# Kernel tuning notes

Measured on AMD Instinct MI355X. Metric: run time of the kernel, lower is better.

Reference implementation:

```python
import jax, jax.numpy as jnp
import numpy as np

LEAKY_SLOPE = 0.2  # tf.nn.leaky_relu default alpha
L2_EPS = 1e-12     # tf.nn.l2_normalize default epsilon


def setup_inputs() -> dict:
    key = jax.random.key(0)
    N, d, E, k = 100000, 64, 1600000, 3
    k0, k1, k2, k3 = jax.random.split(key, 4)
    x = jax.random.normal(k0, (N, d), dtype=jnp.float32)
    edge_index = jax.random.randint(k1, (2, E), 0, N, dtype=jnp.int32)
    scale = 1.0 / np.sqrt(d).astype(np.float32)
    W_gcn = jax.random.normal(k2, (k, d, d), dtype=jnp.float32) * scale
    W_int = jax.random.normal(k3, (k, d, d), dtype=jnp.float32) * scale
    b_gcn = jnp.zeros((k, d), dtype=jnp.float32)
    b_int = jnp.zeros((k, d), dtype=jnp.float32)
    return {"x": x, "edge_index": edge_index, "W_gcn": W_gcn, "b_gcn": b_gcn,
            "W_int": W_int, "b_int": b_int}


def _l2norm(h):
    sq = jnp.sum(h * h, axis=-1, keepdims=True)
    return h * jax.lax.rsqrt(jnp.maximum(sq, L2_EPS))


def reference(x, edge_index, W_gcn, b_gcn, W_int, b_int):
    N = x.shape[0]
    row, col = edge_index[0], edge_index[1]
    # LightGCN.norm_adj: symmetric normalization D^-1/2 A D^-1/2 (no self-loops)
    deg = jax.ops.segment_sum(jnp.ones_like(row, dtype=x.dtype), row, num_segments=N)
    dinv = jnp.where(deg > 0, jax.lax.rsqrt(deg), 0.0)
    w = dinv[row] * dinv[col]  # [E]

    def agg(h):
        # sparse normed_adj @ h : gather source feats, scale, scatter-add to dst
        return jax.ops.segment_sum(w[:, None] * h[col], row, num_segments=N)

    lrelu = lambda z: jax.nn.leaky_relu(z, LEAKY_SLOPE)
    h = x
    outs = [x]
    for i in range(W_gcn.shape[0]):
        ha = agg(h)  # [N, d]
        h = lrelu(ha @ W_gcn[i] + b_gcn[i]) + lrelu((h * ha) @ W_int[i] + b_int[i])
        outs.append(_l2norm(h))
    return jnp.concatenate(outs, axis=-1)  # [N, (k+1)*d]
```

## Files before the change

### kernel.cpp

```cpp
#include <hip/hip_runtime.h>


#define LEAKY 0.2f
#define NBK_MAX 512
#define TILE_A 4096
#define BCAP 5120

typedef unsigned short ushort_t;
typedef short short8 __attribute__((ext_vector_type(8)));
typedef float f32x4 __attribute__((ext_vector_type(4)));

__device__ __forceinline__ float lrelu(float z) { return z > 0.f ? z : LEAKY * z; }

__device__ __forceinline__ unsigned f2bf(float f) {
  unsigned u = __float_as_uint(f);
  return (u + 0x7FFFu + ((u >> 16) & 1u)) >> 16;
}

__device__ __forceinline__ float bf2f(unsigned u) {
  return __uint_as_float(u << 16);
}

__device__ __forceinline__ int rfl(const int* p) {
  return __builtin_amdgcn_readfirstlane(*p);
}

__global__ __launch_bounds__(256) void zerotails_k(int* __restrict__ tails, int nbk) {
  int t = blockIdx.x * 256 + threadIdx.x;
  if (t < nbk) tails[t] = 0;
}

__global__ __launch_bounds__(256) void bucket_k(const int* __restrict__ row,
                                                const int* __restrict__ col,
                                                int* __restrict__ tails,
                                                unsigned int* __restrict__ buckets,
                                                int E, int nbk) {
  __shared__ int bcnt[NBK_MAX], bex[NBK_MAX], bnext[NBK_MAX], gbase[NBK_MAX];
  __shared__ int ssc[256];
  int t = threadIdx.x;
  int ts = blockIdx.x * TILE_A;
  int tn = E - ts;
  if (tn > TILE_A) tn = TILE_A;
  bcnt[t] = 0;
  bcnt[t + 256] = 0;
  __syncthreads();
  for (int i = t; i < tn; i += 256) atomicAdd(&bcnt[row[ts + i] >> 8], 1);
  __syncthreads();
  int a0 = bcnt[2 * t], a1 = bcnt[2 * t + 1];
  ssc[t] = a0 + a1;
  __syncthreads();
  #pragma unroll
  for (int off = 1; off < 256; off <<= 1) {
    int x = (t >= off) ? ssc[t - off] : 0;
    __syncthreads();
    ssc[t] += x;
    __syncthreads();
  }
  int ex = ssc[t] - (a0 + a1);
  bex[2 * t] = ex;
  bex[2 * t + 1] = ex + a0;
  bnext[2 * t] = ex;
  bnext[2 * t + 1] = ex + a0;
  if (t < nbk && bcnt[t] > 0) gbase[t] = atomicAdd(&tails[t], bcnt[t]);
  int t2 = t + 256;
  if (t2 < nbk && bcnt[t2] > 0) gbase[t2] = atomicAdd(&tails[t2], bcnt[t2]);
  __syncthreads();
  for (int i = t; i < tn; i += 256) {
    int r = row[ts + i], c = col[ts + i];
    int b = r >> 8;
    int k = atomicAdd(&bnext[b], 1) - bex[b];
    int pos = gbase[b] + k;
    if (pos < BCAP)
      buckets[(size_t)b * BCAP + pos] = ((unsigned)(r & 255) << 24) | (unsigned)c;
  }
}

__global__ __launch_bounds__(512) void bkscan_k(const int* __restrict__ tails,
                                                int* __restrict__ bkbase,
                                                int* __restrict__ rp,
                                                int nbk, int N, int E) {
  __shared__ int s[512];
  int t = threadIdx.x;
  int v = (t < nbk) ? tails[t] : 0;
  s[t] = v;
  __syncthreads();
  #pragma unroll
  for (int off = 1; off < 512; off <<= 1) {
    int x = (t >= off) ? s[t - off] : 0;
    __syncthreads();
    s[t] += x;
    __syncthreads();
  }
  if (t < nbk) bkbase[t] = s[t] - v;
  if (t == 0) rp[N] = E;
}

__global__ __launch_bounds__(256) void csr_k(const int* __restrict__ tails,
                                             const int* __restrict__ bkbase,
                                             const unsigned int* __restrict__ buckets,
                                             int* __restrict__ rp,
                                             float* __restrict__ dinv,
                                             int* __restrict__ packed, int N) {
  __shared__ int cnt[256], sc[256], cnt2[256];
  int b = blockIdx.x, t = threadIdx.x;
  int row0 = b << 8;
  int nrows = N - row0;
  if (nrows > 256) nrows = 256;
  int cb = tails[b];
  if (cb > BCAP) cb = BCAP;
  int base = bkbase[b];
  const unsigned int* ent = buckets + (size_t)b * BCAP;
  cnt[t] = 0;
  __syncthreads();
  for (int i = t; i < cb; i += 256) atomicAdd(&cnt[ent[i] >> 24], 1);
  __syncthreads();
  int v = cnt[t];
  sc[t] = v;
  __syncthreads();
  #pragma unroll
  for (int off = 1; off < 256; off <<= 1) {
    int x = (t >= off) ? sc[t - off] : 0;
    __syncthreads();
    sc[t] += x;
    __syncthreads();
  }
  int ex = sc[t] - v;
  if (t < nrows) {
    rp[row0 + t] = base + ex;
    dinv[row0 + t] = (v > 0) ? rsqrtf((float)v) : 0.f;
  }
  cnt[t] = ex;
  cnt2[t] = 0;
  __syncthreads();
  for (int i = t; i < cb; i += 256) {
    unsigned e = ent[i];
    int rl = e >> 24;
    int slot = atomicAdd(&cnt2[rl], 1);
    packed[base + cnt[rl] + slot] = (int)(e & 0xFFFFFFu);
  }
}

__global__ __launch_bounds__(256) void copyx_k(const float* __restrict__ x,
                                               const float* __restrict__ dinv,
                                               float* __restrict__ out,
                                               ushort_t* __restrict__ xb,
                                               ushort_t* __restrict__ xg,
                                               int N, int ostride4) {
  int total = N * 16;
  int stride = gridDim.x * blockDim.x;
  for (int i = blockIdx.x * blockDim.x + threadIdx.x; i < total; i += stride) {
    int n = i >> 4, c4 = i & 15;
    float4 v = ((const float4*)x)[i];
    ((float4*)out)[(size_t)n * ostride4 + c4] = v;
    unsigned p0 = f2bf(v.x) | (f2bf(v.y) << 16);
    unsigned p1 = f2bf(v.z) | (f2bf(v.w) << 16);
    ((uint2*)xb)[i] = make_uint2(p0, p1);
    float dv = dinv[n];
    unsigned q0 = f2bf(v.x * dv) | (f2bf(v.y * dv) << 16);
    unsigned q1 = f2bf(v.z * dv) | (f2bf(v.w * dv) << 16);
    ((uint2*)xg)[i] = make_uint2(q0, q1);
  }
}

__global__ __launch_bounds__(256) void packw_k(const float* __restrict__ Wg,
                                               const float* __restrict__ Wi,
                                               ushort_t* __restrict__ Wfrag,
                                               int total) {
  int tid = blockIdx.x * 256 + threadIdx.x;
  if (tid >= total) return;
  int lane = tid & 63;
  int kh = (tid >> 6) & 1;
  int nt = (tid >> 7) & 3;
  int gm = (tid >> 9) & 1;
  int ly = tid >> 10;
  const float* W = (gm ? Wi : Wg) + (size_t)ly * 4096;
  int kb = (kh << 5) + ((lane >> 4) << 3);
  int n = (nt << 4) + (lane & 15);
  unsigned u[4];
  #pragma unroll
  for (int j = 0; j < 4; ++j) {
    unsigned lo = f2bf(W[(kb + 2 * j) * 64 + n]);
    unsigned hi = f2bf(W[(kb + 2 * j + 1) * 64 + n]);
    u[j] = lo | (hi << 16);
  }
  ((uint4*)Wfrag)[tid] = make_uint4(u[0], u[1], u[2], u[3]);
}

__global__ __launch_bounds__(256) void agg_k(const int* __restrict__ rp,
                                             const int* __restrict__ packed,
                                             const float* __restrict__ dinv,
                                             const ushort_t* __restrict__ gin,
                                             ushort_t* __restrict__ ha, int N) {
  int wv = (((blockIdx.x << 2) + (threadIdx.x >> 6)) << 1);
  if (wv >= N) return;
  int lane = threadIdx.x & 63;
  int grp = lane >> 3;
  int l8 = lane & 7;
  bool have1 = (wv + 1) < N;
  int s0 = rfl(&rp[wv]);
  int e0 = rfl(&rp[wv + 1]);
  int s1 = have1 ? rfl(&rp[wv + 1]) : 0;
  int e1 = have1 ? rfl(&rp[wv + 2]) : 0;
  float dr0 = __int_as_float(__builtin_amdgcn_readfirstlane(__float_as_int(dinv[wv])));
  float dr1 = have1 ? __int_as_float(__builtin_amdgcn_readfirstlane(
                          __float_as_int(dinv[wv + 1])))
                    : 0.f;
  float a0[8], a1[8];
  #pragma unroll
  for (int i = 0; i < 8; ++i) { a0[i] = 0.f; a1[i] = 0.f; }
  int bidx0 = grp << 2;
  int ch0 = s0, ch1 = s1;
  while (ch0 < e0 || ch1 < e1) {
    int m0 = e0 - ch0;
    if (m0 > 64) m0 = 64;
    int m1 = e1 - ch1;
    if (m1 > 64) m1 = 64;
    int cl0 = (m0 > 0 && lane < m0) ? packed[ch0 + lane] : 0;
    int cl1 = (m1 > 0 && lane < m1) ? packed[ch1 + lane] : 0;
    int mm = m0 > m1 ? m0 : m1;
    int nit = (mm + 7) >> 3;
    #pragma unroll 2
    for (int j = 0; j < nit; ++j) {
      int bi = bidx0 + (j << 5);
      int c0 = __builtin_amdgcn_ds_bpermute(bi, cl0);
      int c1 = __builtin_amdgcn_ds_bpermute(bi, cl1);
      int eidx = (j << 3) + grp;
      float msk0 = (eidx < m0) ? 1.f : 0.f;
      float msk1 = (eidx < m1) ? 1.f : 0.f;
      uint4 v0 = ((const uint4*)(gin + ((size_t)c0 << 6)))[l8];
      uint4 v1 = ((const uint4*)(gin + ((size_t)c1 << 6)))[l8];
      a0[0] = fmaf(msk0, bf2f(v0.x & 0xFFFFu), a0[0]);
      a0[1] = fmaf(msk0, bf2f(v0.x >> 16), a0[1]);
      a0[2] = fmaf(msk0, bf2f(v0.y & 0xFFFFu), a0[2]);
      a0[3] = fmaf(msk0, bf2f(v0.y >> 16), a0[3]);
      a0[4] = fmaf(msk0, bf2f(v0.z & 0xFFFFu), a0[4]);
      a0[5] = fmaf(msk0, bf2f(v0.z >> 16), a0[5]);
      a0[6] = fmaf(msk0, bf2f(v0.w & 0xFFFFu), a0[6]);
      a0[7] = fmaf(msk0, bf2f(v0.w >> 16), a0[7]);
      a1[0] = fmaf(msk1, bf2f(v1.x & 0xFFFFu), a1[0]);
      a1[1] = fmaf(msk1, bf2f(v1.x >> 16), a1[1]);
      a1[2] = fmaf(msk1, bf2f(v1.y & 0xFFFFu), a1[2]);
      a1[3] = fmaf(msk1, bf2f(v1.y >> 16), a1[3]);
      a1[4] = fmaf(msk1, bf2f(v1.z & 0xFFFFu), a1[4]);
      a1[5] = fmaf(msk1, bf2f(v1.z >> 16), a1[5]);
      a1[6] = fmaf(msk1, bf2f(v1.w & 0xFFFFu), a1[6]);
      a1[7] = fmaf(msk1, bf2f(v1.w >> 16), a1[7]);
    }
    ch0 += 64;
    ch1 += 64;
  }
  #pragma unroll
  for (int off = 8; off < 64; off <<= 1)
    #pragma unroll
    for (int i = 0; i < 8; ++i) {
      a0[i] += __shfl_xor(a0[i], off);
      a1[i] += __shfl_xor(a1[i], off);
    }
  if (grp == 0) {
    unsigned u0 = f2bf(a0[0] * dr0) | (f2bf(a0[1] * dr0) << 16);
    unsigned u1 = f2bf(a0[2] * dr0) | (f2bf(a0[3] * dr0) << 16);
    unsigned u2 = f2bf(a0[4] * dr0) | (f2bf(a0[5] * dr0) << 16);
    unsigned u3 = f2bf(a0[6] * dr0) | (f2bf(a0[7] * dr0) << 16);
    ((uint4*)(ha + ((size_t)wv << 6)))[l8] = make_uint4(u0, u1, u2, u3);
  } else if (grp == 1 && have1) {
    unsigned u0 = f2bf(a1[0] * dr1) | (f2bf(a1[1] * dr1) << 16);
    unsigned u1 = f2bf(a1[2] * dr1) | (f2bf(a1[3] * dr1) << 16);
    unsigned u2 = f2bf(a1[4] * dr1) | (f2bf(a1[5] * dr1) << 16);
    unsigned u3 = f2bf(a1[6] * dr1) | (f2bf(a1[7] * dr1) << 16);
    ((uint4*)(ha + ((size_t)(wv + 1) << 6)))[l8] = make_uint4(u0, u1, u2, u3);
  }
}

__global__ __launch_bounds__(256) void gemmM_k(const ushort_t* __restrict__ ha,
                                               const ushort_t* __restrict__ hin,
                                               const ushort_t* __restrict__ Wfrag,
                                               const float* __restrict__ bg,
                                               const float* __restrict__ bi,
                                               const float* __restrict__ dinv,
                                               ushort_t* __restrict__ hout,
                                               ushort_t* __restrict__ gout,
                                               float* __restrict__ outp,
                                               int N, int ntiles, int ostride) {
  int lane = threadIdx.x & 63;
  int gq = lane >> 4, ln15 = lane & 15;
  const short8* wf = (const short8*)Wfrag;
  short8 bG[8], bI[8];
  #pragma unroll
  for (int nt = 0; nt < 4; ++nt)
    #pragma unroll
    for (int kh = 0; kh < 2; ++kh) {
      bG[nt * 2 + kh] = wf[nt * 128 + kh * 64 + lane];
      bI[nt * 2 + kh] = wf[512 + nt * 128 + kh * 64 + lane];
    }
  float bgv[4], biv[4];
  #pragma unroll
  for (int nt = 0; nt < 4; ++nt) {
    bgv[nt] = bg[nt * 16 + ln15];
    biv[nt] = bi[nt * 16 + ln15];
  }
  int wid = (blockIdx.x << 2) + (threadIdx.x >> 6);
  int nw = gridDim.x << 2;
  for (int tile = wid; tile < ntiles; tile += nw) {
    int node0 = tile << 4;
    const short8* pa =
        (const short8*)(ha + (size_t)(node0 + ln15) * 64 + gq * 8);
    const short8* ph =
        (const short8*)(hin + (size_t)(node0 + ln15) * 64 + gq * 8);
    f32x4 acc1[4], acc2[4];
    #pragma unroll
    for (int nt = 0; nt < 4; ++nt) {
      acc1[nt] = (f32x4){bgv[nt], bgv[nt], bgv[nt], bgv[nt]};
      acc2[nt] = (f32x4){biv[nt], biv[nt], biv[nt], biv[nt]};
    }
    #pragma unroll
    for (int kh = 0; kh < 2; ++kh) {
      short8 af = pa[kh * 4];
      short8 hf = ph[kh * 4];
      short8 vmf;
      #pragma unroll
      for (int e2 = 0; e2 < 8; ++e2) {
        float fa = bf2f((ushort_t)af[e2]);
        float fh = bf2f((ushort_t)hf[e2]);
        vmf[e2] = (short)f2bf(fa * fh);
      }
      #pragma unroll
      for (int nt = 0; nt < 4; ++nt) {
        acc1[nt] = __builtin_amdgcn_mfma_f32_16x16x32_bf16(af, bG[nt * 2 + kh],
                                                           acc1[nt], 0, 0, 0);
        acc2[nt] = __builtin_amdgcn_mfma_f32_16x16x32_bf16(vmf, bI[nt * 2 + kh],
                                                           acc2[nt], 0, 0, 0);
      }
    }
    float z[4][4];
    float ssr[4] = {0.f, 0.f, 0.f, 0.f};
    #pragma unroll
    for (int nt = 0; nt < 4; ++nt)
      #pragma unroll
      for (int reg = 0; reg < 4; ++reg) {
        float zz = lrelu(acc1[nt][reg]) + lrelu(acc2[nt][reg]);
        z[nt][reg] = zz;
        ssr[reg] = fmaf(zz, zz, ssr[reg]);
      }
    #pragma unroll
    for (int off = 1; off < 16; off <<= 1)
      #pragma unroll
      for (int reg = 0; reg < 4; ++reg) ssr[reg] += __shfl_xor(ssr[reg], off);
    float inv[4];
    #pragma unroll
    for (int reg = 0; reg < 4; ++reg)
      inv[reg] = rsqrtf(fmaxf(ssr[reg], 1e-12f));
    #pragma unroll
    for (int reg = 0; reg < 4; ++reg) {
      int r = node0 + 4 * gq + reg;
      if (r < N) {
        float dv = dinv[r];
        #pragma unroll
        for (int nt = 0; nt < 4; ++nt) {
          outp[(size_t)r * ostride + nt * 16 + ln15] = z[nt][reg] * inv[reg];
          hout[(size_t)r * 64 + nt * 16 + ln15] = (ushort_t)f2bf(z[nt][reg]);
          gout[(size_t)r * 64 + nt * 16 + ln15] =
              (ushort_t)f2bf(z[nt][reg] * dv);
        }
      }
    }
  }
}

extern "C" void kernel_launch(void* const* d_in, const int* in_sizes, int n_in,
                              void* d_out, int out_size, void* d_ws, size_t ws_size,
                              hipStream_t stream) {
  const float* x  = (const float*)d_in[0];
  const int*   ei = (const int*)d_in[1];
  const float* Wg = (const float*)d_in[2];
  const float* bg = (const float*)d_in[3];
  const float* Wi = (const float*)d_in[4];
  const float* bi = (const float*)d_in[5];
  float* out = (float*)d_out;

  const int d = 64;
  const int N = in_sizes[0] / d;
  const int E = in_sizes[1] / 2;
  const int K = in_sizes[2] / (d * d);
  const int* row = ei;
  const int* col = ei + E;
  const int nbk = (N + 255) / 256;
  const int N16 = (N + 15) & ~15;
  const int ntiles = N16 / 16;
  const int ostride = (K + 1) * d;

  char* ws = (char*)d_ws;
  size_t off = 0;
  auto alloc = [&](size_t bytes) {
    char* p = ws + off;
    off = (off + bytes + 255) & ~(size_t)255;
    return p;
  };
  int*   tails  = (int*)alloc((size_t)NBK_MAX * 4);
  int*   bkbase = (int*)alloc((size_t)NBK_MAX * 4);
  int*   rp     = (int*)alloc((size_t)(N + 1) * 4);
  float* dinv   = (float*)alloc((size_t)N * 4);
  unsigned int* buckets = (unsigned int*)alloc((size_t)nbk * BCAP * 4);
  int*   packed = (int*)alloc((size_t)E * 4);
  ushort_t* ha  = (ushort_t*)alloc((size_t)N16 * d * 2);
  ushort_t* hb0 = (ushort_t*)alloc((size_t)N16 * d * 2);
  ushort_t* hb1 = (ushort_t*)alloc((size_t)N16 * d * 2);
  ushort_t* xb  = (ushort_t*)alloc((size_t)N16 * d * 2);
  ushort_t* hg0 = (ushort_t*)alloc((size_t)N16 * d * 2);
  ushort_t* hg1 = (ushort_t*)alloc((size_t)N16 * d * 2);
  ushort_t* xg  = (ushort_t*)alloc((size_t)N16 * d * 2);
  ushort_t* Wfrag = (ushort_t*)alloc((size_t)K * 8192 * 2);
  (void)ws_size;

  zerotails_k<<<(nbk + 255) / 256, 256, 0, stream>>>(tails, nbk);
  int ntA = (E + TILE_A - 1) / TILE_A;
  bucket_k<<<ntA, 256, 0, stream>>>(row, col, tails, buckets, E, nbk);
  bkscan_k<<<1, 512, 0, stream>>>(tails, bkbase, rp, nbk, N, E);
  csr_k<<<nbk, 256, 0, stream>>>(tails, bkbase, buckets, rp, dinv, packed, N);
  copyx_k<<<2048, 256, 0, stream>>>(x, dinv, out, xb, xg, N, ostride / 4);
  int wtotal = K * 1024;
  packw_k<<<(wtotal + 255) / 256, 256, 0, stream>>>(Wg, Wi, Wfrag, wtotal);

  const ushort_t* hin = xb;
  const ushort_t* gin = xg;
  ushort_t* hbufs[2] = {hb0, hb1};
  ushort_t* gbufs[2] = {hg0, hg1};
  int aggblocks = (N + 7) / 8;
  for (int i = 0; i < K; ++i) {
    ushort_t* hout = hbufs[i & 1];
    ushort_t* gout = gbufs[i & 1];
    agg_k<<<aggblocks, 256, 0, stream>>>(rp, packed, dinv, gin, ha, N);
    gemmM_k<<<1024, 256, 0, stream>>>(
        ha, hin, Wfrag + (size_t)i * 8192, bg + (size_t)i * d,
        bi + (size_t)i * d, dinv, hout, gout, out + (size_t)(i + 1) * d,
        N, ntiles, ostride);
    hin = hout;
    gin = gout;
  }
}
```

Baseline: 229.7 us.

## Drop unscaled bf16 h buffers, recover h from scaled copy, fuse x copy into CSR

The unscaled bf16 feature buffer is no longer stored. The GEMM kernel rebuilds h by multiplying the dinv-scaled copy by 1/dinv, which removes one bf16 write per layer and one read. The x copy and bf16 conversion move into csr_k, which uses a shared-memory dinv, so copyx_k and its extra launch go away. The edge-bucketing tile size doubles and the GEMM grid is sized to one tile per wave. The risks are extra rounding error from the bf16 round trip through scaling, and zero-degree rows losing their h value (rdv=0), which changes the h*ha term for nodes that have no out-edges.

After: 231.4 us. Within noise of the previous version (+0.8%).

```diff
diff --git a/kernel.cpp b/kernel.cpp
--- a/kernel.cpp
+++ b/kernel.cpp
@@ -3,7 +3,7 @@
 
 #define LEAKY 0.2f
 #define NBK_MAX 512
-#define TILE_A 4096
+#define TILE_A 8192
 #define BCAP 5120
 
 typedef unsigned short ushort_t;
@@ -100,8 +100,13 @@
                                              const unsigned int* __restrict__ buckets,
                                              int* __restrict__ rp,
                                              float* __restrict__ dinv,
-                                             int* __restrict__ packed, int N) {
+                                             int* __restrict__ packed,
+                                             const float* __restrict__ x,
+                                             float* __restrict__ out,
+                                             ushort_t* __restrict__ xg,
+                                             int N, int ostride4) {
   __shared__ int cnt[256], sc[256], cnt2[256];
+  __shared__ float sdinv[256];
   int b = blockIdx.x, t = threadIdx.x;
   int row0 = b << 8;
   int nrows = N - row0;
@@ -119,15 +124,17 @@
   __syncthreads();
   #pragma unroll
   for (int off = 1; off < 256; off <<= 1) {
-    int x = (t >= off) ? sc[t - off] : 0;
-    __syncthreads();
-    sc[t] += x;
+    int x2 = (t >= off) ? sc[t - off] : 0;
+    __syncthreads();
+    sc[t] += x2;
     __syncthreads();
   }
   int ex = sc[t] - v;
+  float dvv = (v > 0) ? rsqrtf((float)v) : 0.f;
+  sdinv[t] = dvv;
   if (t < nrows) {
     rp[row0 + t] = base + ex;
-    dinv[row0 + t] = (v > 0) ? rsqrtf((float)v) : 0.f;
+    dinv[row0 + t] = dvv;
   }
   cnt[t] = ex;
   cnt2[t] = 0;
@@ -138,27 +145,16 @@
     int slot = atomicAdd(&cnt2[rl], 1);
     packed[base + cnt[rl] + slot] = (int)(e & 0xFFFFFFu);
   }
-}
-
-__global__ __launch_bounds__(256) void copyx_k(const float* __restrict__ x,
-                                               const float* __restrict__ dinv,
-                                               float* __restrict__ out,
-                                               ushort_t* __restrict__ xb,
-                                               ushort_t* __restrict__ xg,
-                                               int N, int ostride4) {
-  int total = N * 16;
-  int stride = gridDim.x * blockDim.x;
-  for (int i = blockIdx.x * blockDim.x + threadIdx.x; i < total; i += stride) {
-    int n = i >> 4, c4 = i & 15;
-    float4 v = ((const float4*)x)[i];
-    ((float4*)out)[(size_t)n * ostride4 + c4] = v;
-    unsigned p0 = f2bf(v.x) | (f2bf(v.y) << 16);
-    unsigned p1 = f2bf(v.z) | (f2bf(v.w) << 16);
-    ((uint2*)xb)[i] = make_uint2(p0, p1);
-    float dv = dinv[n];
-    unsigned q0 = f2bf(v.x * dv) | (f2bf(v.y * dv) << 16);
-    unsigned q1 = f2bf(v.z * dv) | (f2bf(v.w * dv) << 16);
-    ((uint2*)xg)[i] = make_uint2(q0, q1);
+  int base4 = row0 << 4;
+  int tot4 = nrows << 4;
+  for (int i = t; i < tot4; i += 256) {
+    int rl = i >> 4, c4 = i & 15;
+    float4 vx = ((const float4*)x)[base4 + i];
+    ((float4*)out)[(size_t)(row0 + rl) * ostride4 + c4] = vx;
+    float dv = sdinv[rl];
+    unsigned q0 = f2bf(vx.x * dv) | (f2bf(vx.y * dv) << 16);
+    unsigned q1 = f2bf(vx.z * dv) | (f2bf(vx.w * dv) << 16);
+    ((uint2*)xg)[base4 + i] = make_uint2(q0, q1);
   }
 }
 
@@ -272,12 +268,11 @@
 }
 
 __global__ __launch_bounds__(256) void gemmM_k(const ushort_t* __restrict__ ha,
-                                               const ushort_t* __restrict__ hin,
+                                               const ushort_t* __restrict__ gin,
                                                const ushort_t* __restrict__ Wfrag,
                                                const float* __restrict__ bg,
                                                const float* __restrict__ bi,
                                                const float* __restrict__ dinv,
-                                               ushort_t* __restrict__ hout,
                                                ushort_t* __restrict__ gout,
                                                float* __restrict__ outp,
                                                int N, int ntiles, int ostride) {
@@ -302,10 +297,11 @@
   int nw = gridDim.x << 2;
   for (int tile = wid; tile < ntiles; tile += nw) {
     int node0 = tile << 4;
-    const short8* pa =
-        (const short8*)(ha + (size_t)(node0 + ln15) * 64 + gq * 8);
-    const short8* ph =
-        (const short8*)(hin + (size_t)(node0 + ln15) * 64 + gq * 8);
+    int r15 = node0 + ln15;
+    float dnv = dinv[r15];
+    float rdv = (dnv > 0.f) ? 1.f / dnv : 0.f;
+    const short8* pa = (const short8*)(ha + (size_t)r15 * 64 + gq * 8);
+    const short8* ph = (const short8*)(gin + (size_t)r15 * 64 + gq * 8);
     f32x4 acc1[4], acc2[4];
     #pragma unroll
     for (int nt = 0; nt < 4; ++nt) {
@@ -315,12 +311,12 @@
     #pragma unroll
     for (int kh = 0; kh < 2; ++kh) {
       short8 af = pa[kh * 4];
-      short8 hf = ph[kh * 4];
+      short8 gf = ph[kh * 4];
       short8 vmf;
       #pragma unroll
       for (int e2 = 0; e2 < 8; ++e2) {
         float fa = bf2f((ushort_t)af[e2]);
-        float fh = bf2f((ushort_t)hf[e2]);
+        float fh = bf2f((ushort_t)gf[e2]) * rdv;
         vmf[e2] = (short)f2bf(fa * fh);
       }
       #pragma unroll
@@ -357,7 +353,6 @@
         #pragma unroll
         for (int nt = 0; nt < 4; ++nt) {
           outp[(size_t)r * ostride + nt * 16 + ln15] = z[nt][reg] * inv[reg];
-          hout[(size_t)r * 64 + nt * 16 + ln15] = (ushort_t)f2bf(z[nt][reg]);
           gout[(size_t)r * 64 + nt * 16 + ln15] =
               (ushort_t)f2bf(z[nt][reg] * dv);
         }
@@ -398,13 +393,10 @@
   int*   tails  = (int*)alloc((size_t)NBK_MAX * 4);
   int*   bkbase = (int*)alloc((size_t)NBK_MAX * 4);
   int*   rp     = (int*)alloc((size_t)(N + 1) * 4);
-  float* dinv   = (float*)alloc((size_t)N * 4);
+  float* dinv   = (float*)alloc((size_t)N16 * 4);
   unsigned int* buckets = (unsigned int*)alloc((size_t)nbk * BCAP * 4);
   int*   packed = (int*)alloc((size_t)E * 4);
   ushort_t* ha  = (ushort_t*)alloc((size_t)N16 * d * 2);
-  ushort_t* hb0 = (ushort_t*)alloc((size_t)N16 * d * 2);
-  ushort_t* hb1 = (ushort_t*)alloc((size_t)N16 * d * 2);
-  ushort_t* xb  = (ushort_t*)alloc((size_t)N16 * d * 2);
   ushort_t* hg0 = (ushort_t*)alloc((size_t)N16 * d * 2);
   ushort_t* hg1 = (ushort_t*)alloc((size_t)N16 * d * 2);
   ushort_t* xg  = (ushort_t*)alloc((size_t)N16 * d * 2);
@@ -415,25 +407,22 @@
   int ntA = (E + TILE_A - 1) / TILE_A;
   bucket_k<<<ntA, 256, 0, stream>>>(row, col, tails, buckets, E, nbk);
   bkscan_k<<<1, 512, 0, stream>>>(tails, bkbase, rp, nbk, N, E);
-  csr_k<<<nbk, 256, 0, stream>>>(tails, bkbase, buckets, rp, dinv, packed, N);
-  copyx_k<<<2048, 256, 0, stream>>>(x, dinv, out, xb, xg, N, ostride / 4);
+  csr_k<<<nbk, 256, 0, stream>>>(tails, bkbase, buckets, rp, dinv, packed,
+                                 x, out, xg, N, ostride / 4);
   int wtotal = K * 1024;
   packw_k<<<(wtotal + 255) / 256, 256, 0, stream>>>(Wg, Wi, Wfrag, wtotal);
 
-  const ushort_t* hin = xb;
   const ushort_t* gin = xg;
-  ushort_t* hbufs[2] = {hb0, hb1};
   ushort_t* gbufs[2] = {hg0, hg1};
   int aggblocks = (N + 7) / 8;
+  int gemmblocks = (ntiles + 3) / 4;
   for (int i = 0; i < K; ++i) {
-    ushort_t* hout = hbufs[i & 1];
     ushort_t* gout = gbufs[i & 1];
     agg_k<<<aggblocks, 256, 0, stream>>>(rp, packed, dinv, gin, ha, N);
-    gemmM_k<<<1024, 256, 0, stream>>>(
-        ha, hin, Wfrag + (size_t)i * 8192, bg + (size_t)i * d,
-        bi + (size_t)i * d, dinv, hout, gout, out + (size_t)(i + 1) * d,
+    gemmM_k<<<gemmblocks, 256, 0, stream>>>(
+        ha, gin, Wfrag + (size_t)i * 8192, bg + (size_t)i * d,
+        bi + (size_t)i * d, dinv, gout, out + (size_t)(i + 1) * d,
         N, ntiles, ostride);
-    hin = hout;
     gin = gout;
   }
 }
```

## Store gathered neighbor features in FP8 to halve aggregation gather bandwidth

Applied to the files above, without the earlier changes.

The dinv-scaled feature copies that the aggregation kernel gathers per edge are now stored as FP8 (e4m3) instead of bf16. The kernel decodes them with packed FP8-to-float conversions, which halves the bytes fetched per random row gather. The last layer skips writing the gather buffer because no later layer reads it. The tail-zeroing kernel is folded into the weight-packing kernel to save a launch. The main risk is accuracy: FP8 gives about 3 mantissa bits and a limited range, which may exceed the output tolerance.

Result: faster. 223.7 us (-2.6%).

```diff
diff --git a/kernel.cpp b/kernel.cpp
--- a/kernel.cpp
+++ b/kernel.cpp
@@ -7,8 +7,10 @@
 #define BCAP 5120
 
 typedef unsigned short ushort_t;
+typedef unsigned char uchar_t;
 typedef short short8 __attribute__((ext_vector_type(8)));
 typedef float f32x4 __attribute__((ext_vector_type(4)));
+typedef float f32x2 __attribute__((ext_vector_type(2)));
 
 __device__ __forceinline__ float lrelu(float z) { return z > 0.f ? z : LEAKY * z; }
 
@@ -21,13 +23,12 @@
   return __uint_as_float(u << 16);
 }
 
+__device__ __forceinline__ unsigned f2fp8(float f) {
+  return (unsigned)__builtin_amdgcn_cvt_pk_fp8_f32(f, f, 0, false) & 0xFFu;
+}
+
 __device__ __forceinline__ int rfl(const int* p) {
   return __builtin_amdgcn_readfirstlane(*p);
-}
-
-__global__ __launch_bounds__(256) void zerotails_k(int* __restrict__ tails, int nbk) {
-  int t = blockIdx.x * 256 + threadIdx.x;
-  if (t < nbk) tails[t] = 0;
 }
 
 __global__ __launch_bounds__(256) void bucket_k(const int* __restrict__ row,
@@ -144,7 +145,7 @@
                                                const float* __restrict__ dinv,
                                                float* __restrict__ out,
                                                ushort_t* __restrict__ xb,
-                                               ushort_t* __restrict__ xg,
+                                               uchar_t* __restrict__ xg,
                                                int N, int ostride4) {
   int total = N * 16;
   int stride = gridDim.x * blockDim.x;
@@ -156,17 +157,21 @@
     unsigned p1 = f2bf(v.z) | (f2bf(v.w) << 16);
     ((uint2*)xb)[i] = make_uint2(p0, p1);
     float dv = dinv[n];
-    unsigned q0 = f2bf(v.x * dv) | (f2bf(v.y * dv) << 16);
-    unsigned q1 = f2bf(v.z * dv) | (f2bf(v.w * dv) << 16);
-    ((uint2*)xg)[i] = make_uint2(q0, q1);
+    unsigned pkA =
+        (unsigned)__builtin_amdgcn_cvt_pk_fp8_f32(v.x * dv, v.y * dv, 0, false);
+    unsigned pkB =
+        (unsigned)__builtin_amdgcn_cvt_pk_fp8_f32(v.z * dv, v.w * dv, 0, false);
+    ((unsigned*)xg)[i] = (pkA & 0xFFFFu) | ((pkB & 0xFFFFu) << 16);
   }
 }
 
 __global__ __launch_bounds__(256) void packw_k(const float* __restrict__ Wg,
                                                const float* __restrict__ Wi,
                                                ushort_t* __restrict__ Wfrag,
-                                               int total) {
+                                               int total,
+                                               int* __restrict__ tails, int nbk) {
   int tid = blockIdx.x * 256 + threadIdx.x;
+  if (tid < nbk) tails[tid] = 0;
   if (tid >= total) return;
   int lane = tid & 63;
   int kh = (tid >> 6) & 1;
@@ -189,7 +194,7 @@
 __global__ __launch_bounds__(256) void agg_k(const int* __restrict__ rp,
                                              const int* __restrict__ packed,
                                              const float* __restrict__ dinv,
-                                             const ushort_t* __restrict__ gin,
+                                             const uchar_t* __restrict__ gin,
                                              ushort_t* __restrict__ ha, int N) {
   int wv = (((blockIdx.x << 2) + (threadIdx.x >> 6)) << 1);
   if (wv >= N) return;
@@ -227,24 +232,25 @@
       int eidx = (j << 3) + grp;
       float msk0 = (eidx < m0) ? 1.f : 0.f;
       float msk1 = (eidx < m1) ? 1.f : 0.f;
-      uint4 v0 = ((const uint4*)(gin + ((size_t)c0 << 6)))[l8];
-      uint4 v1 = ((const uint4*)(gin + ((size_t)c1 << 6)))[l8];
-      a0[0] = fmaf(msk0, bf2f(v0.x & 0xFFFFu), a0[0]);
-      a0[1] = fmaf(msk0, bf2f(v0.x >> 16), a0[1]);
-      a0[2] = fmaf(msk0, bf2f(v0.y & 0xFFFFu), a0[2]);
-      a0[3] = fmaf(msk0, bf2f(v0.y >> 16), a0[3]);
-      a0[4] = fmaf(msk0, bf2f(v0.z & 0xFFFFu), a0[4]);
-      a0[5] = fmaf(msk0, bf2f(v0.z >> 16), a0[5]);
-      a0[6] = fmaf(msk0, bf2f(v0.w & 0xFFFFu), a0[6]);
-      a0[7] = fmaf(msk0, bf2f(v0.w >> 16), a0[7]);
-      a1[0] = fmaf(msk1, bf2f(v1.x & 0xFFFFu), a1[0]);
-      a1[1] = fmaf(msk1, bf2f(v1.x >> 16), a1[1]);
-      a1[2] = fmaf(msk1, bf2f(v1.y & 0xFFFFu), a1[2]);
-      a1[3] = fmaf(msk1, bf2f(v1.y >> 16), a1[3]);
-      a1[4] = fmaf(msk1, bf2f(v1.z & 0xFFFFu), a1[4]);
-      a1[5] = fmaf(msk1, bf2f(v1.z >> 16), a1[5]);
-      a1[6] = fmaf(msk1, bf2f(v1.w & 0xFFFFu), a1[6]);
-      a1[7] = fmaf(msk1, bf2f(v1.w >> 16), a1[7]);
+      uint2 v0 = ((const uint2*)(gin + ((size_t)c0 << 6)))[l8];
+      uint2 v1 = ((const uint2*)(gin + ((size_t)c1 << 6)))[l8];
+      f32x2 d;
+      d = __builtin_amdgcn_cvt_pk_f32_fp8((int)v0.x, false);
+      a0[0] = fmaf(msk0, d[0], a0[0]);  a0[1] = fmaf(msk0, d[1], a0[1]);
+      d = __builtin_amdgcn_cvt_pk_f32_fp8((int)v0.x, true);
+      a0[2] = fmaf(msk0, d[0], a0[2]);  a0[3] = fmaf(msk0, d[1], a0[3]);
+      d = __builtin_amdgcn_cvt_pk_f32_fp8((int)v0.y, false);
+      a0[4] = fmaf(msk0, d[0], a0[4]);  a0[5] = fmaf(msk0, d[1], a0[5]);
+      d = __builtin_amdgcn_cvt_pk_f32_fp8((int)v0.y, true);
+      a0[6] = fmaf(msk0, d[0], a0[6]);  a0[7] = fmaf(msk0, d[1], a0[7]);
+      d = __builtin_amdgcn_cvt_pk_f32_fp8((int)v1.x, false);
+      a1[0] = fmaf(msk1, d[0], a1[0]);  a1[1] = fmaf(msk1, d[1], a1[1]);
+      d = __builtin_amdgcn_cvt_pk_f32_fp8((int)v1.x, true);
+      a1[2] = fmaf(msk1, d[0], a1[2]);  a1[3] = fmaf(msk1, d[1], a1[3]);
+      d = __builtin_amdgcn_cvt_pk_f32_fp8((int)v1.y, false);
+      a1[4] = fmaf(msk1, d[0], a1[4]);  a1[5] = fmaf(msk1, d[1], a1[5]);
+      d = __builtin_amdgcn_cvt_pk_f32_fp8((int)v1.y, true);
+      a1[6] = fmaf(msk1, d[0], a1[6]);  a1[7] = fmaf(msk1, d[1], a1[7]);
     }
     ch0 += 64;
     ch1 += 64;
@@ -278,9 +284,10 @@
                                                const float* __restrict__ bi,
                                                const float* __restrict__ dinv,
                                                ushort_t* __restrict__ hout,
-                                               ushort_t* __restrict__ gout,
+                                               uchar_t* __restrict__ gout,
                                                float* __restrict__ outp,
-                                               int N, int ntiles, int ostride) {
+                                               int N, int ntiles, int ostride,
+                                               int writeg) {
   int lane = threadIdx.x & 63;
   int gq = lane >> 4, ln15 = lane & 15;
   const short8* wf = (const short8*)Wfrag;
@@ -358,8 +365,9 @@
         for (int nt = 0; nt < 4; ++nt) {
           outp[(size_t)r * ostride + nt * 16 + ln15] = z[nt][reg] * inv[reg];
           hout[(size_t)r * 64 + nt * 16 + ln15] = (ushort_t)f2bf(z[nt][reg]);
-          gout[(size_t)r * 64 + nt * 16 + ln15] =
-              (ushort_t)f2bf(z[nt][reg] * dv);
+          if (writeg)
+            gout[(size_t)r * 64 + nt * 16 + ln15] =
+                (uchar_t)f2fp8(z[nt][reg] * dv);
         }
       }
     }
@@ -398,41 +406,41 @@
   int*   tails  = (int*)alloc((size_t)NBK_MAX * 4);
   int*   bkbase = (int*)alloc((size_t)NBK_MAX * 4);
   int*   rp     = (int*)alloc((size_t)(N + 1) * 4);
-  float* dinv   = (float*)alloc((size_t)N * 4);
+  float* dinv   = (float*)alloc((size_t)N16 * 4);
   unsigned int* buckets = (unsigned int*)alloc((size_t)nbk * BCAP * 4);
   int*   packed = (int*)alloc((size_t)E * 4);
   ushort_t* ha  = (ushort_t*)alloc((size_t)N16 * d * 2);
   ushort_t* hb0 = (ushort_t*)alloc((size_t)N16 * d * 2);
   ushort_t* hb1 = (ushort_t*)alloc((size_t)N16 * d * 2);
   ushort_t* xb  = (ushort_t*)alloc((size_t)N16 * d * 2);
-  ushort_t* hg0 = (ushort_t*)alloc((size_t)N16 * d * 2);
-  ushort_t* hg1 = (ushort_t*)alloc((size_t)N16 * d * 2);
-  ushort_t* xg  = (ushort_t*)alloc((size_t)N16 * d * 2);
+  uchar_t* hg0  = (uchar_t*)alloc((size_t)N16 * d);
+  uchar_t* hg1  = (uchar_t*)alloc((size_t)N16 * d);
+  uchar_t* xg   = (uchar_t*)alloc((size_t)N16 * d);
   ushort_t* Wfrag = (ushort_t*)alloc((size_t)K * 8192 * 2);
   (void)ws_size;
 
-  zerotails_k<<<(nbk + 255) / 256, 256, 0, stream>>>(tails, nbk);
+  int wtotal = K * 1024;
+  packw_k<<<(wtotal + 255) / 256, 256, 0, stream>>>(Wg, Wi, Wfrag, wtotal,
+                                                    tails, nbk);
   int ntA = (E + TILE_A - 1) / TILE_A;
   bucket_k<<<ntA, 256, 0, stream>>>(row, col, tails, buckets, E, nbk);
   bkscan_k<<<1, 512, 0, stream>>>(tails, bkbase, rp, nbk, N, E);
   csr_k<<<nbk, 256, 0, stream>>>(tails, bkbase, buckets, rp, dinv, packed, N);
   copyx_k<<<2048, 256, 0, stream>>>(x, dinv, out, xb, xg, N, ostride / 4);
-  int wtotal = K * 1024;
-  packw_k<<<(wtotal + 255) / 256, 256, 0, stream>>>(Wg, Wi, Wfrag, wtotal);
 
   const ushort_t* hin = xb;
-  const ushort_t* gin = xg;
+  const uchar_t* gin = xg;
   ushort_t* hbufs[2] = {hb0, hb1};
-  ushort_t* gbufs[2] = {hg0, hg1};
+  uchar_t* gbufs[2] = {hg0, hg1};
   int aggblocks = (N + 7) / 8;
   for (int i = 0; i < K; ++i) {
     ushort_t* hout = hbufs[i & 1];
-    ushort_t* gout = gbufs[i & 1];
+    uchar_t* gout = gbufs[i & 1];
     agg_k<<<aggblocks, 256, 0, stream>>>(rp, packed, dinv, gin, ha, N);
     gemmM_k<<<1024, 256, 0, stream>>>(
         ha, hin, Wfrag + (size_t)i * 8192, bg + (size_t)i * d,
         bi + (size_t)i * d, dinv, hout, gout, out + (size_t)(i + 1) * d,
-        N, ntiles, ostride);
+        N, ntiles, ostride, (i + 1 < K) ? 1 : 0);
     hin = hout;
     gin = gout;
   }
```
